# Optimization experiments

Measured on AMD Instinct MI355X. Metric: run time of the kernel, lower is better.

## Reference

```python
import jax, jax.numpy as jnp
import numpy as np

def _round_ste(x):
    # StraightThrough: forward = round, backward = identity
    return x + jax.lax.stop_gradient(jnp.round(x) - x)

def setup_inputs() -> dict:
    key = jax.random.key(0)
    k1, k2, k3, k4, k5 = jax.random.split(key, 5)
    in_f, out_f, n_tok = 4096, 4096, 8192
    return {
        "input": jax.random.normal(k1, (n_tok, in_f), dtype=jnp.float32),
        "weight": jax.random.normal(k2, (out_f, in_f), dtype=jnp.float32),
        "bias": jax.random.normal(k3, (out_f,), dtype=jnp.float32),
        "w_scale": jax.random.uniform(k4, (1,), dtype=jnp.float32),
        "b_scale": jax.random.uniform(k5, (1,), dtype=jnp.float32),
    }

def reference(input, weight, bias, w_scale, b_scale):
    # straight-through rounding of quantized latents (use_straight_through=True, compress_bias=True)
    w_q = _round_ste(weight)
    b_q = _round_ste(bias)
    # decoder: per-tensor affine dequantization
    w_dec = w_scale * w_q          # [out, in]
    b_dec = b_scale * b_q          # [out]
    # F.linear: input @ weight.T + bias
    return jnp.einsum('ni,oi->no', input, w_dec) + b_dec
```

## Files before the change

### kernel.cpp

```cpp
#include <hip/hip_runtime.h>
#include <stdint.h>


using bf16x8   = __attribute__((ext_vector_type(8))) __bf16;
using floatx16 = __attribute__((ext_vector_type(16))) float;
using us8      = __attribute__((ext_vector_type(8))) unsigned short;
using us4      = __attribute__((ext_vector_type(4))) unsigned short;

__device__ __forceinline__ unsigned short f2bf_rne(float x) {
    unsigned int u = __float_as_uint(x);
    return (unsigned short)((u + 0x7fffu + ((u >> 16) & 1u)) >> 16);
}

__device__ __forceinline__ void load_lds16(const unsigned short* g, unsigned short* l) {
    __builtin_amdgcn_global_load_lds(
        (__attribute__((address_space(1))) void*)g,
        (__attribute__((address_space(3))) void*)l,
        16, 0, 0);
}

__global__ __launch_bounds__(256) void cvt_both(
    const float* __restrict__ inA, unsigned short* __restrict__ outA, long long nA4,
    const float* __restrict__ inB, unsigned short* __restrict__ outB, long long nB4) {
    const long long i = (long long)blockIdx.x * 256 + threadIdx.x;
    if (i < nA4) {
        float4 v = ((const float4*)inA)[i];
        us4 o = { f2bf_rne(v.x), f2bf_rne(v.y), f2bf_rne(v.z), f2bf_rne(v.w) };
        ((us4*)outA)[i] = o;
    } else {
        const long long j = i - nA4;
        if (j < nB4) {
            float4 v = ((const float4*)inB)[j];
            us4 o = { f2bf_rne(rintf(v.x)), f2bf_rne(rintf(v.y)),
                      f2bf_rne(rintf(v.z)), f2bf_rne(rintf(v.w)) };
            ((us4*)outB)[j] = o;
        }
    }
}

__global__ __launch_bounds__(256) void gemm_bf16_bt(
    const unsigned short* __restrict__ A,
    const unsigned short* __restrict__ B,
    const float* __restrict__ bias,
    const float* __restrict__ wscale_p,
    const float* __restrict__ bscale_p,
    float* __restrict__ C,
    int M, int N, int K) {
    constexpr int BM = 128, BK = 64;
    __shared__ unsigned short ldsA[BM * BK];
    __shared__ unsigned short ldsB[BM * BK];

    const int tid  = threadIdx.x;
    const int wave = tid >> 6;
    const int lane = tid & 63;

    const int bm = blockIdx.y * BM;
    const int bn = blockIdx.x * BM;
    const int wm = (wave >> 1) * 64;
    const int wn = (wave & 1) * 64;

    const float wsc = wscale_p[0];
    const float bsc = bscale_p[0];

    const int col = lane & 31;
    const int khalf = lane >> 5;

    float badd[2];
#pragma unroll
    for (int ni = 0; ni < 2; ++ni)
        badd[ni] = bsc * rintf(bias[bn + wn + ni * 32 + col]);

    const int g_st = ((lane & 7) ^ (lane >> 3)) * 8;
    const unsigned short* gAp[4];
    const unsigned short* gBp[4];
    unsigned short* lA[4];
    unsigned short* lB[4];
#pragma unroll
    for (int i = 0; i < 4; ++i) {
        const int r = wave * 32 + i * 8 + (lane >> 3);
        gAp[i] = A + (size_t)(bm + r) * K + g_st;
        gBp[i] = B + (size_t)(bn + r) * K + g_st;
        lA[i] = &ldsA[(wave * 256 + i * 64) * 8];
        lB[i] = &ldsB[(wave * 256 + i * 64) * 8];
    }

    floatx16 acc[2][2] = {};

    for (int kt = 0; kt < K; kt += BK) {
#pragma unroll
        for (int i = 0; i < 4; ++i) {
            load_lds16(gAp[i] + kt, lA[i]);
            load_lds16(gBp[i] + kt, lB[i]);
        }
        __syncthreads();

#pragma unroll
        for (int ks = 0; ks < 4; ++ks) {
            const int gc = ks * 2 + khalf;
            const int slot = (gc ^ (lane & 7)) * 8;
            bf16x8 af[2], bfr[2];
#pragma unroll
            for (int mi = 0; mi < 2; ++mi) {
                const int off = (wm + mi * 32 + col) * BK + slot;
                af[mi] = __builtin_bit_cast(bf16x8, *(const us8*)&ldsA[off]);
            }
#pragma unroll
            for (int ni = 0; ni < 2; ++ni) {
                const int off = (wn + ni * 32 + col) * BK + slot;
                bfr[ni] = __builtin_bit_cast(bf16x8, *(const us8*)&ldsB[off]);
            }
#pragma unroll
            for (int mi = 0; mi < 2; ++mi)
#pragma unroll
                for (int ni = 0; ni < 2; ++ni)
                    acc[mi][ni] = __builtin_amdgcn_mfma_f32_32x32x16_bf16(
                        af[mi], bfr[ni], acc[mi][ni], 0, 0, 0);
        }
        __syncthreads();
    }

    const int rbase = 4 * khalf;
#pragma unroll
    for (int mi = 0; mi < 2; ++mi) {
#pragma unroll
        for (int ni = 0; ni < 2; ++ni) {
            const int n = bn + wn + ni * 32 + col;
#pragma unroll
            for (int reg = 0; reg < 16; ++reg) {
                const int m = bm + wm + mi * 32 + (reg & 3) + 8 * (reg >> 2) + rbase;
                C[(size_t)m * N + n] = acc[mi][ni][reg] * wsc + badd[ni];
            }
        }
    }
}

__global__ __launch_bounds__(256) void fallback_gemm(
    const float* __restrict__ A, const float* __restrict__ W,
    const float* __restrict__ bias, const float* __restrict__ wsp,
    const float* __restrict__ bsp, float* __restrict__ C, int M, int N, int K) {
    const int n = blockIdx.x * 256 + threadIdx.x;
    const int m = blockIdx.y;
    if (n >= N || m >= M) return;
    float s = 0.f;
    for (int k = 0; k < K; ++k)
        s += A[(size_t)m * K + k] * rintf(W[(size_t)n * K + k]);
    C[(size_t)m * N + n] = s * wsp[0] + bsp[0] * rintf(bias[n]);
}

extern "C" void kernel_launch(void* const* d_in, const int* in_sizes, int n_in,
                              void* d_out, int out_size, void* d_ws, size_t ws_size,
                              hipStream_t stream) {
    const float* input  = (const float*)d_in[0];
    const float* weight = (const float*)d_in[1];
    const float* bias   = (const float*)d_in[2];
    const float* wscale = (const float*)d_in[3];
    const float* bscale = (const float*)d_in[4];
    float* out = (float*)d_out;

    const int N = in_sizes[2];
    const int K = in_sizes[1] / N;
    const int M = in_sizes[0] / K;

    const size_t needA = (size_t)M * K * sizeof(unsigned short);
    const size_t needB = (size_t)N * K * sizeof(unsigned short);

    if (ws_size >= needA + needB && (M % 128) == 0 && (N % 128) == 0 &&
        (K % 64) == 0) {
        unsigned short* Abf = (unsigned short*)d_ws;
        unsigned short* Bbf = (unsigned short*)((char*)d_ws + needA);
        const long long nA4 = (long long)M * K / 4;
        const long long nB4 = (long long)N * K / 4;
        const long long nthr = nA4 + nB4;
        cvt_both<<<(unsigned)((nthr + 255) / 256), 256, 0, stream>>>(
            input, Abf, nA4, weight, Bbf, nB4);
        dim3 grid(N / 128, M / 128);
        gemm_bf16_bt<<<grid, 256, 0, stream>>>(Abf, Bbf, bias, wscale, bscale, out, M, N, K);
    } else {
        dim3 grid((N + 255) / 256, M);
        fallback_gemm<<<grid, 256, 0, stream>>>(input, weight, bias, wscale, bscale, out, M, N, K);
    }
}
```

Measured before the change: 532.1 us.

## Add 256x256 double-buffered bf16 GEMM with interleaved staging and XCD block remap

Adds a new 512-thread GEMM kernel with 256x256 output tiles, double-buffered LDS staging, global loads interleaved between MFMA phases, s_setprio around MFMA bursts, and a workgroup index remap that spreads consecutive blocks across the 8 XCDs. It replaces the single-buffered 128x128 kernel, which syncs around every K step, whenever the shapes divide evenly. The goal is to overlap memory with compute, raise data reuse per tile and improve L2 locality. In exchange it needs 128KB of LDS per block and more registers per wave, which limits occupancy to one block per CU.

```diff
diff --git a/kernel.cpp b/kernel.cpp
--- a/kernel.cpp
+++ b/kernel.cpp
@@ -12,7 +12,7 @@
     return (unsigned short)((u + 0x7fffu + ((u >> 16) & 1u)) >> 16);
 }
 
-__device__ __forceinline__ void load_lds16(const unsigned short* g, unsigned short* l) {
+__device__ __forceinline__ void stage16(const unsigned short* g, unsigned short* l) {
     __builtin_amdgcn_global_load_lds(
         (__attribute__((address_space(1))) void*)g,
         (__attribute__((address_space(3))) void*)l,
@@ -38,6 +38,163 @@
     }
 }
 
+__global__ __launch_bounds__(512) void gemm256_8ph(
+    const unsigned short* __restrict__ A,
+    const unsigned short* __restrict__ B,
+    const float* __restrict__ bias,
+    const float* __restrict__ wscale_p,
+    const float* __restrict__ bscale_p,
+    float* __restrict__ C,
+    int M, int N, int K) {
+    constexpr int BK   = 64;
+    constexpr int TILE = 256 * BK;
+    __shared__ unsigned short ldsA[2 * TILE];
+    __shared__ unsigned short ldsB[2 * TILE];
+
+    const int tid  = threadIdx.x;
+    const int wave = tid >> 6;
+    const int lane = tid & 63;
+
+    const int nbx = N >> 8;
+    int wg;
+    {
+        const int cpx = (int)gridDim.x >> 3;
+        wg = ((int)blockIdx.x & 7) * cpx + ((int)blockIdx.x >> 3);
+    }
+    const int bm = (wg / nbx) << 8;
+    const int bn = (wg % nbx) << 8;
+
+    const int wm    = (wave >> 2) << 7;
+    const int wn    = (wave & 3) << 6;
+    const int col   = lane & 31;
+    const int khalf = lane >> 5;
+
+    const int row512 = tid >> 3;
+    const int gk = ((tid & 7) ^ (row512 & 7)) << 3;
+    const unsigned short* gA = A + (size_t)(bm + row512) * K + gk;
+    const unsigned short* gB = B + (size_t)(bn + row512) * K + gk;
+    unsigned short* sA = ldsA + (wave << 9);
+    unsigned short* sB = ldsB + (wave << 9);
+
+    int rowA[4], rowB[2], slotv[4];
+#pragma unroll
+    for (int mi = 0; mi < 4; ++mi) rowA[mi] = (wm + mi * 32 + col) << 6;
+#pragma unroll
+    for (int ni = 0; ni < 2; ++ni) rowB[ni] = (wn + ni * 32 + col) << 6;
+#pragma unroll
+    for (int ks = 0; ks < 4; ++ks) slotv[ks] = ((ks * 2 + khalf) ^ (col & 7)) << 3;
+
+    const float wsc = wscale_p[0];
+    const float bsc = bscale_p[0];
+    float badd[2];
+#pragma unroll
+    for (int ni = 0; ni < 2; ++ni)
+        badd[ni] = bsc * rintf(bias[bn + wn + ni * 32 + col]);
+
+    const int NT = K >> 6;
+
+#pragma unroll
+    for (int i = 0; i < 4; ++i) {
+        stage16(gA + (size_t)(i * 64) * K,      sA + i * 4096);
+        stage16(gB + (size_t)(i * 64) * K,      sB + i * 4096);
+    }
+#pragma unroll
+    for (int i = 0; i < 4; ++i) {
+        stage16(gA + (size_t)(i * 64) * K + 64, sA + TILE + i * 4096);
+        stage16(gB + (size_t)(i * 64) * K + 64, sB + TILE + i * 4096);
+    }
+    asm volatile("s_waitcnt vmcnt(8)" ::: "memory");
+    __builtin_amdgcn_s_barrier();
+    __builtin_amdgcn_sched_barrier(0);
+
+    floatx16 acc[4][2] = {};
+
+#define READ_KS(ks, ar, br)                                                       \
+    {                                                                             \
+        const int so = slotv[ks];                                                 \
+        _Pragma("unroll") for (int mi = 0; mi < 4; ++mi)                          \
+            ar[mi] = __builtin_bit_cast(bf16x8, *(const us8*)&SA[rowA[mi] + so]); \
+        _Pragma("unroll") for (int ni = 0; ni < 2; ++ni)                          \
+            br[ni] = __builtin_bit_cast(bf16x8, *(const us8*)&SB[rowB[ni] + so]); \
+    }
+
+#define MFMA8(ar, br)                                                             \
+    __builtin_amdgcn_s_setprio(1);                                                \
+    _Pragma("unroll") for (int mi = 0; mi < 4; ++mi)                              \
+        _Pragma("unroll") for (int ni = 0; ni < 2; ++ni)                          \
+            acc[mi][ni] = __builtin_amdgcn_mfma_f32_32x32x16_bf16(                \
+                ar[mi], br[ni], acc[mi][ni], 0, 0, 0);                            \
+    __builtin_amdgcn_s_setprio(0);
+
+    for (int t = 0; t < NT; ++t) {
+        const unsigned short* SA = ldsA + (t & 1) * TILE;
+        const unsigned short* SB = ldsB + (t & 1) * TILE;
+        unsigned short* dA = sA + (t & 1) * TILE;
+        unsigned short* dB = sB + (t & 1) * TILE;
+        const size_t kt2 = (size_t)(t + 2) * BK;
+        const bool do_stage = (t + 2 < NT);
+
+        bf16x8 a0[4], a1[4], a2[4], a3[4];
+        bf16x8 b0[2], b1[2], b2[2], b3[2];
+
+        READ_KS(0, a0, b0)
+        READ_KS(1, a1, b1)
+        MFMA8(a0, b0)
+        __builtin_amdgcn_sched_barrier(0);
+
+        READ_KS(2, a2, b2)
+        READ_KS(3, a3, b3)
+        MFMA8(a1, b1)
+
+        asm volatile("s_waitcnt lgkmcnt(0)" ::: "memory");
+        __builtin_amdgcn_sched_barrier(0);
+        __builtin_amdgcn_s_barrier();
+        __builtin_amdgcn_sched_barrier(0);
+
+        if (do_stage) {
+#pragma unroll
+            for (int i = 0; i < 2; ++i) {
+                stage16(gA + (size_t)(i * 64) * K + kt2, dA + i * 4096);
+                stage16(gB + (size_t)(i * 64) * K + kt2, dB + i * 4096);
+            }
+        }
+        MFMA8(a2, b2)
+        __builtin_amdgcn_sched_barrier(0);
+
+        if (do_stage) {
+#pragma unroll
+            for (int i = 2; i < 4; ++i) {
+                stage16(gA + (size_t)(i * 64) * K + kt2, dA + i * 4096);
+                stage16(gB + (size_t)(i * 64) * K + kt2, dB + i * 4096);
+            }
+        }
+        MFMA8(a3, b3)
+        __builtin_amdgcn_sched_barrier(0);
+
+        if (do_stage)         { asm volatile("s_waitcnt vmcnt(8)" ::: "memory"); }
+        else if (t + 2 == NT) { asm volatile("s_waitcnt vmcnt(0)" ::: "memory"); }
+        __builtin_amdgcn_s_barrier();
+        __builtin_amdgcn_sched_barrier(0);
+    }
+
+#undef READ_KS
+#undef MFMA8
+
+    const int rb = khalf << 2;
+#pragma unroll
+    for (int mi = 0; mi < 4; ++mi) {
+#pragma unroll
+        for (int ni = 0; ni < 2; ++ni) {
+            const int n = bn + wn + ni * 32 + col;
+#pragma unroll
+            for (int reg = 0; reg < 16; ++reg) {
+                const int m = bm + wm + mi * 32 + (reg & 3) + 8 * (reg >> 2) + rb;
+                C[(size_t)m * N + n] = acc[mi][ni][reg] * wsc + badd[ni];
+            }
+        }
+    }
+}
+
 __global__ __launch_bounds__(256) void gemm_bf16_bt(
     const unsigned short* __restrict__ A,
     const unsigned short* __restrict__ B,
@@ -89,8 +246,8 @@
     for (int kt = 0; kt < K; kt += BK) {
 #pragma unroll
         for (int i = 0; i < 4; ++i) {
-            load_lds16(gAp[i] + kt, lA[i]);
-            load_lds16(gBp[i] + kt, lB[i]);
+            stage16(gAp[i] + kt, lA[i]);
+            stage16(gBp[i] + kt, lB[i]);
         }
         __syncthreads();
 
@@ -173,8 +330,17 @@
         const long long nthr = nA4 + nB4;
         cvt_both<<<(unsigned)((nthr + 255) / 256), 256, 0, stream>>>(
             input, Abf, nA4, weight, Bbf, nB4);
-        dim3 grid(N / 128, M / 128);
-        gemm_bf16_bt<<<grid, 256, 0, stream>>>(Abf, Bbf, bias, wscale, bscale, out, M, N, K);
+
+        const int nwg256 = (M / 256) * (N / 256);
+        if ((M % 256) == 0 && (N % 256) == 0 && (K / 64) >= 4 &&
+            (nwg256 % 8) == 0) {
+            gemm256_8ph<<<dim3(nwg256), 512, 0, stream>>>(
+                Abf, Bbf, bias, wscale, bscale, out, M, N, K);
+        } else {
+            dim3 grid(N / 128, M / 128);
+            gemm_bf16_bt<<<grid, 256, 0, stream>>>(Abf, Bbf, bias, wscale,
+                                                   bscale, out, M, N, K);
+        }
     } else {
         dim3 grid((N + 255) / 256, M);
         fallback_gemm<<<grid, 256, 0, stream>>>(input, weight, bias, wscale, bscale, out, M, N, K);
```

Result: slower. 553.4 us (+4.0%).
